# Kernel optimization log

Measured on AMD Instinct MI355X. Metric: run time of the kernel, lower is better.

## Reference

```python
import jax, jax.numpy as jnp
import numpy as np

N = 50000      # num_nodes
E = 1000000    # graph edges
EP = 400000    # pos/neg link-pred edges
H = 128        # hidden_dim
C = 768        # chemical_dim
L = 2          # num GCN layers


def setup_inputs() -> dict:
    key = jax.random.key(0)
    ks = jax.random.split(key, 12)
    edge_index = jax.random.randint(ks[0], (2, E), 0, N)
    chemistry = jax.random.normal(ks[1], (N, C), jnp.float32)
    pos_edge = jax.random.randint(ks[2], (EP, 2), 0, N)
    neg_edge = jax.random.randint(ks[3], (EP, 2), 0, N)
    smiles_mask = jax.random.uniform(ks[4], (N,), jnp.float32)
    node_emb = jax.random.normal(ks[5], (N, H), jnp.float32) * 0.1
    conv_w = jax.random.normal(ks[6], (L, H, H), jnp.float32) / np.sqrt(H)
    conv_b = jnp.zeros((L, H), jnp.float32)
    chem_w = jax.random.normal(ks[7], (C, H), jnp.float32) / np.sqrt(C)
    chem_b = jnp.zeros((H,), jnp.float32)
    dec_w1 = jax.random.normal(ks[8], (2 * H, H), jnp.float32) / np.sqrt(2 * H)
    dec_b1 = jnp.zeros((H,), jnp.float32)
    dec_w2 = jax.random.normal(ks[9], (H, 1), jnp.float32) / np.sqrt(H)
    dec_b2 = jnp.zeros((1,), jnp.float32)
    return dict(edge_index=edge_index, chemistry=chemistry, pos_edge=pos_edge,
                neg_edge=neg_edge, smiles_mask=smiles_mask, node_emb=node_emb,
                conv_w=conv_w, conv_b=conv_b, chem_w=chem_w, chem_b=chem_b,
                dec_w1=dec_w1, dec_b1=dec_b1, dec_w2=dec_w2, dec_b2=dec_b2)


def reference(edge_index, chemistry, pos_edge, neg_edge, smiles_mask, node_emb,
              conv_w, conv_b, chem_w, chem_b, dec_w1, dec_b1, dec_w2, dec_b2):
    row, col = edge_index[0], edge_index[1]  # src -> dst
    # GCN symmetric normalization (add_self_loops=False)
    deg = jax.ops.segment_sum(jnp.ones((E,), jnp.float32), col, num_segments=N)
    dinv = jnp.where(deg > 0, 1.0 / jnp.sqrt(jnp.maximum(deg, 1.0)), 0.0)
    norm = dinv[row] * dinv[col]  # [E]

    # Encoder: structure-only GCN over learned node embeddings
    z = node_emb
    for l in range(L):
        h = z @ conv_w[l]                       # [N,H]
        msg = h[row] * norm[:, None]            # gather [E,H]
        agg = jax.ops.segment_sum(msg, col, num_segments=N)  # scatter-add
        z = jax.nn.relu(agg + conv_b[l])

    # Chemistry projection, masked by smiles validity
    c = jax.nn.relu(chemistry @ chem_w + chem_b) * smiles_mask[:, None]  # [N,H]

    def decode(edges):
        src, dst = edges[:, 0], edges[:, 1]
        f = jnp.concatenate([z[src] * z[dst], c[src] * c[dst]], axis=-1)  # [Ep,2H]
        hmid = jax.nn.relu(f @ dec_w1 + dec_b1)
        return (hmid @ dec_w2 + dec_b2)[:, 0]

    return decode(pos_edge), decode(neg_edge)
```

## Files before the change

### kernel.cpp

```cpp
#include <hip/hip_runtime.h>
#include <hip/hip_fp16.h>

#define NN 50000
#define NE 1000000
#define NEP 400000
#define HD 128
#define CD 768
#define NB_SCAN 196
#define FSTR 256
#define NBKT 196
#define PBLK 2048
#define NPB ((2 * NEP + PBLK - 1) / PBLK)

typedef _Float16 f16x8 __attribute__((ext_vector_type(8)));
typedef _Float16 f16x2 __attribute__((ext_vector_type(2)));
typedef __fp16 hf16x2 __attribute__((ext_vector_type(2)));
typedef __attribute__((ext_vector_type(4))) float f32x4;

__device__ __forceinline__ unsigned pk2h(float a, float b) {
    hf16x2 p = __builtin_amdgcn_cvt_pkrtz(a, b);
    return __builtin_bit_cast(unsigned, p);
}
__device__ __forceinline__ ushort f2h(float x) {
    return (ushort)(pk2h(x, 0.f) & 0xffffu);
}
__device__ __forceinline__ unsigned h2mul(unsigned a, unsigned b) {
    f16x2 ha = __builtin_bit_cast(f16x2, a);
    f16x2 hb = __builtin_bit_cast(f16x2, b);
    f16x2 r = ha * hb;
    return __builtin_bit_cast(unsigned, r);
}
__device__ __forceinline__ f16x8 pack8h(float4 a0, float4 a1) {
    union { unsigned u[4]; f16x8 v; } r;
    r.u[0] = pk2h(a0.x, a0.y);
    r.u[1] = pk2h(a0.z, a0.w);
    r.u[2] = pk2h(a1.x, a1.y);
    r.u[3] = pk2h(a1.z, a1.w);
    return r.v;
}
__device__ __forceinline__ float2 h2f2(unsigned u) {
    f16x2 h = __builtin_bit_cast(f16x2, u);
    return make_float2((float)h[0], (float)h[1]);
}

__global__ __launch_bounds__(256) void count_kernel(const int* __restrict__ col,
                                                    int* __restrict__ cnt) {
    int i = blockIdx.x * 256 + threadIdx.x;
    if (i < NE) atomicAdd(&cnt[col[i]], 1);
}

__global__ __launch_bounds__(256) void scan1_kernel(const int* __restrict__ cnt,
                                                    int* __restrict__ partial,
                                                    int* __restrict__ bsum,
                                                    float* __restrict__ dinv) {
    __shared__ int s[256];
    int i = blockIdx.x * 256 + threadIdx.x;
    int v = (i < NN) ? cnt[i] : 0;
    if (i < NN) dinv[i] = (v > 0) ? 1.0f / sqrtf((float)v) : 0.0f;
    s[threadIdx.x] = v;
    __syncthreads();
    for (int o = 1; o < 256; o <<= 1) {
        int t = (threadIdx.x >= o) ? s[threadIdx.x - o] : 0;
        __syncthreads();
        s[threadIdx.x] += t;
        __syncthreads();
    }
    if (i < NN) partial[i] = s[threadIdx.x] - v;
    if (threadIdx.x == 255) bsum[blockIdx.x] = s[255];
}

__global__ __launch_bounds__(256) void scan2_kernel(int* __restrict__ bsum) {
    __shared__ int s[256];
    int v = (threadIdx.x < NB_SCAN) ? bsum[threadIdx.x] : 0;
    s[threadIdx.x] = v;
    __syncthreads();
    for (int o = 1; o < 256; o <<= 1) {
        int t = (threadIdx.x >= o) ? s[threadIdx.x - o] : 0;
        __syncthreads();
        s[threadIdx.x] += t;
        __syncthreads();
    }
    if (threadIdx.x < NB_SCAN) bsum[threadIdx.x] = s[threadIdx.x] - v;
}

__global__ __launch_bounds__(256) void scan3_kernel(const int* __restrict__ partial,
                                                    const int* __restrict__ bsum,
                                                    int* __restrict__ off,
                                                    int* __restrict__ cursor) {
    int i = blockIdx.x * 256 + threadIdx.x;
    if (i < NN) {
        int o = partial[i] + bsum[blockIdx.x];
        off[i] = o;
        cursor[i] = o;
    }
}

__global__ __launch_bounds__(256) void fill_kernel(const int* __restrict__ row,
                                                   const int* __restrict__ col,
                                                   const float* __restrict__ dinv,
                                                   int* __restrict__ cursor,
                                                   int* __restrict__ csr_idx,
                                                   float* __restrict__ csr_w) {
    int e = blockIdx.x * 256 + threadIdx.x;
    if (e < NE) {
        int c = col[e], r = row[e];
        int slot = atomicAdd(&cursor[c], 1);
        csr_idx[slot] = r;
        csr_w[slot] = dinv[r];
    }
}

__global__ __launch_bounds__(256) void ehist_kernel(const int* __restrict__ pos,
                                                    const int* __restrict__ neg,
                                                    int* __restrict__ bh,
                                                    int* __restrict__ bcnt) {
    __shared__ int h[NBKT];
    const int t = threadIdx.x;
    if (t < NBKT) h[t] = 0;
    __syncthreads();
    const int base = blockIdx.x * PBLK;
#pragma unroll
    for (int j = 0; j < 8; ++j) {
        int i = base + t + j * 256;
        if (i < 2 * NEP) {
            int s = (i < NEP) ? pos[2 * i] : neg[2 * (i - NEP)];
            atomicAdd(&h[s >> 8], 1);
        }
    }
    __syncthreads();
    if (t < NBKT) {
        bh[blockIdx.x * NBKT + t] = h[t];
        if (h[t]) atomicAdd(&bcnt[t], h[t]);
    }
}

__global__ __launch_bounds__(256) void escan_kernel(const int* __restrict__ bcnt,
                                                    int* __restrict__ base) {
    __shared__ int s[256];
    const int t = threadIdx.x;
    int v = (t < NBKT) ? bcnt[t] : 0;
    s[t] = v;
    __syncthreads();
    for (int o = 1; o < 256; o <<= 1) {
        int x = (t >= o) ? s[t - o] : 0;
        __syncthreads();
        s[t] += x;
        __syncthreads();
    }
    if (t < NBKT) base[t] = s[t] - v;
}

__global__ __launch_bounds__(256) void bscan_kernel(const int* __restrict__ bh,
                                                    int* __restrict__ obh) {
    __shared__ int p[256];
    const int b = blockIdx.x;
    const int t = threadIdx.x;
    int v0 = (2 * t < NPB) ? bh[(size_t)(2 * t) * NBKT + b] : 0;
    int v1 = (2 * t + 1 < NPB) ? bh[(size_t)(2 * t + 1) * NBKT + b] : 0;
    p[t] = v0 + v1;
    __syncthreads();
    for (int o = 1; o < 256; o <<= 1) {
        int x = (t >= o) ? p[t - o] : 0;
        __syncthreads();
        p[t] += x;
        __syncthreads();
    }
    int excl = (t > 0) ? p[t - 1] : 0;
    if (2 * t < NPB) obh[(size_t)(2 * t) * NBKT + b] = excl;
    if (2 * t + 1 < NPB) obh[(size_t)(2 * t + 1) * NBKT + b] = excl + v0;
}

__global__ __launch_bounds__(256) void epermute_kernel(const int* __restrict__ pos,
                                                       const int* __restrict__ neg,
                                                       const int* __restrict__ base,
                                                       const int* __restrict__ obh,
                                                       uint2* __restrict__ sd,
                                                       int* __restrict__ oidx) {
    __shared__ int cur[NBKT];
    const int t = threadIdx.x;
    if (t < NBKT) cur[t] = base[t] + obh[(size_t)blockIdx.x * NBKT + t];
    __syncthreads();
    const int bb = blockIdx.x * PBLK;
#pragma unroll
    for (int j = 0; j < 8; ++j) {
        int i = bb + t + j * 256;
        if (i < 2 * NEP) {
            int s, d;
            if (i < NEP) { s = pos[2 * i]; d = pos[2 * i + 1]; }
            else { s = neg[2 * (i - NEP)]; d = neg[2 * (i - NEP) + 1]; }
            int slot = atomicAdd(&cur[s >> 8], 1);
            sd[slot] = make_uint2((unsigned)s, (unsigned)d);
            oidx[slot] = i;
        }
    }
}

__global__ __launch_bounds__(256) void wfrag_all_kernel(const float* __restrict__ w1,
                                                        const float* __restrict__ wc,
                                                        const float* __restrict__ w0,
                                                        const float* __restrict__ wl1,
                                                        ushort* __restrict__ w1f,
                                                        ushort* __restrict__ wcf,
                                                        ushort* __restrict__ wc0f,
                                                        ushort* __restrict__ wc1f) {
    int tid = blockIdx.x * 256 + threadIdx.x;
    int g = tid >> 9;
    const float* w;
    ushort* wf;
    int ks;
    if (g < 8) { w = w1; wf = w1f; ks = g; }
    else if (g < 32) { w = wc; wf = wcf; ks = g - 8; }
    else if (g < 36) { w = w0; wf = wc0f; ks = g - 32; }
    else { w = wl1; wf = wc1f; ks = g - 36; }
    int nt = (tid >> 6) & 7, l = tid & 63;
    int kbase = ks * 32 + ((l >> 4) << 3);
    int colq = nt * 16 + (l & 15);
    ushort r[8];
#pragma unroll
    for (int j = 0; j < 8; ++j) r[j] = f2h(w[(size_t)(kbase + j) * HD + colq]);
    *(uint4*)&wf[(size_t)((ks * 8 + nt) * 64 + l) * 8] = *(uint4*)r;
}

template <int KS, bool EPI>
__global__ __launch_bounds__(256) void feat_mfma_kernel(const float* __restrict__ A,
                                                        const ushort* __restrict__ wf,
                                                        const float* __restrict__ bias,
                                                        const float* __restrict__ mask,
                                                        ushort* __restrict__ out,
                                                        int ostride, int ooff) {
    __shared__ float At[2][64][36];
    const int t = threadIdx.x;
    const int w = t >> 6, lane = t & 63;
    const int rowBase = blockIdx.x * 64;
    const int nt0 = w * 2;
    const int K = KS * 32;

    const int sr0 = t >> 3, sr1 = 32 + (t >> 3), sc4 = (t & 7) * 4;
    const int g0 = rowBase + sr0, g1 = rowBase + sr1;

    float4 p0 = make_float4(0.f, 0.f, 0.f, 0.f), p1 = p0;
    if (g0 < NN) p0 = *(const float4*)&A[(size_t)g0 * K + sc4];
    if (g1 < NN) p1 = *(const float4*)&A[(size_t)g1 * K + sc4];

    f32x4 acc[4][2] = {};

    for (int ks = 0; ks < KS; ++ks) {
        const int b = ks & 1;
        *(float4*)&At[b][sr0][sc4] = p0;
        *(float4*)&At[b][sr1][sc4] = p1;
        __syncthreads();
        if (ks + 1 < KS) {
            p0 = make_float4(0.f, 0.f, 0.f, 0.f); p1 = p0;
            if (g0 < NN) p0 = *(const float4*)&A[(size_t)g0 * K + (ks + 1) * 32 + sc4];
            if (g1 < NN) p1 = *(const float4*)&A[(size_t)g1 * K + (ks + 1) * 32 + sc4];
        }
        f16x8 bf0 = ((const f16x8*)wf)[(ks * 8 + nt0) * 64 + lane];
        f16x8 bf1 = ((const f16x8*)wf)[(ks * 8 + nt0 + 1) * 64 + lane];
#pragma unroll
        for (int mt = 0; mt < 4; ++mt) {
            int row = mt * 16 + (lane & 15);
            float4 a0 = *(const float4*)&At[b][row][(lane >> 4) * 8];
            float4 a1 = *(const float4*)&At[b][row][(lane >> 4) * 8 + 4];
            f16x8 af = pack8h(a0, a1);
            acc[mt][0] = __builtin_amdgcn_mfma_f32_16x16x32_f16(af, bf0, acc[mt][0], 0, 0, 0);
            acc[mt][1] = __builtin_amdgcn_mfma_f32_16x16x32_f16(af, bf1, acc[mt][1], 0, 0, 0);
        }
    }

    const int c0 = lane & 15, rq = lane >> 4;
    float bb0 = EPI ? bias[nt0 * 16 + c0] : 0.f;
    float bb1 = EPI ? bias[nt0 * 16 + 16 + c0] : 0.f;
#pragma unroll
    for (int mt = 0; mt < 4; ++mt) {
#pragma unroll
        for (int reg = 0; reg < 4; ++reg) {
            int grow = rowBase + mt * 16 + rq * 4 + reg;
            if (grow < NN) {
                float v0 = acc[mt][0][reg], v1 = acc[mt][1][reg];
                if (EPI) {
                    float m = mask[grow];
                    v0 = fmaxf(v0 + bb0, 0.f) * m;
                    v1 = fmaxf(v1 + bb1, 0.f) * m;
                }
                out[(size_t)grow * ostride + ooff + nt0 * 16 + c0] = f2h(v0);
                out[(size_t)grow * ostride + ooff + nt0 * 16 + 16 + c0] = f2h(v1);
            }
        }
    }
}

template <bool F16OUT>
__global__ __launch_bounds__(256) void gather_kernel(const int* __restrict__ off,
                                                     const int* __restrict__ cnt,
                                                     const int* __restrict__ csr_idx,
                                                     const float* __restrict__ csr_w,
                                                     const float* __restrict__ dinv,
                                                     const ushort* __restrict__ h,
                                                     const float* __restrict__ bias,
                                                     float* __restrict__ z,
                                                     ushort* __restrict__ zb,
                                                     int ostride) {
    int v = blockIdx.x * 4 + (threadIdx.x >> 6);
    if (v >= NN) return;
    int lane = threadIdx.x & 63;
    int s = off[v];
    int e = s + cnt[v];
    float accx = 0.f, accy = 0.f;
    for (; s + 7 < e; s += 8) {
        int r0 = csr_idx[s], r1 = csr_idx[s + 1], r2 = csr_idx[s + 2], r3 = csr_idx[s + 3];
        int r4 = csr_idx[s + 4], r5 = csr_idx[s + 5], r6 = csr_idx[s + 6], r7 = csr_idx[s + 7];
        unsigned u0 = *(const unsigned*)&h[(size_t)r0 * HD + lane * 2];
        unsigned u1 = *(const unsigned*)&h[(size_t)r1 * HD + lane * 2];
        unsigned u2 = *(const unsigned*)&h[(size_t)r2 * HD + lane * 2];
        unsigned u3 = *(const unsigned*)&h[(size_t)r3 * HD + lane * 2];
        unsigned u4 = *(const unsigned*)&h[(size_t)r4 * HD + lane * 2];
        unsigned u5 = *(const unsigned*)&h[(size_t)r5 * HD + lane * 2];
        unsigned u6 = *(const unsigned*)&h[(size_t)r6 * HD + lane * 2];
        unsigned u7 = *(const unsigned*)&h[(size_t)r7 * HD + lane * 2];
        float w0 = csr_w[s], w1 = csr_w[s + 1], w2 = csr_w[s + 2], w3 = csr_w[s + 3];
        float w4 = csr_w[s + 4], w5 = csr_w[s + 5], w6 = csr_w[s + 6], w7 = csr_w[s + 7];
        float2 f0 = h2f2(u0), f1 = h2f2(u1), f2 = h2f2(u2), f3 = h2f2(u3);
        float2 f4 = h2f2(u4), f5 = h2f2(u5), f6 = h2f2(u6), f7 = h2f2(u7);
        accx = fmaf(f0.x, w0, accx); accy = fmaf(f0.y, w0, accy);
        accx = fmaf(f1.x, w1, accx); accy = fmaf(f1.y, w1, accy);
        accx = fmaf(f2.x, w2, accx); accy = fmaf(f2.y, w2, accy);
        accx = fmaf(f3.x, w3, accx); accy = fmaf(f3.y, w3, accy);
        accx = fmaf(f4.x, w4, accx); accy = fmaf(f4.y, w4, accy);
        accx = fmaf(f5.x, w5, accx); accy = fmaf(f5.y, w5, accy);
        accx = fmaf(f6.x, w6, accx); accy = fmaf(f6.y, w6, accy);
        accx = fmaf(f7.x, w7, accx); accy = fmaf(f7.y, w7, accy);
    }
    for (; s < e; ++s) {
        int r0 = csr_idx[s];
        float w0 = csr_w[s];
        float2 f0 = h2f2(*(const unsigned*)&h[(size_t)r0 * HD + lane * 2]);
        accx = fmaf(f0.x, w0, accx); accy = fmaf(f0.y, w0, accy);
    }
    float dv = dinv[v];
    float2 b = *(const float2*)&bias[lane * 2];
    float ox = fmaxf(fmaf(accx, dv, b.x), 0.f);
    float oy = fmaxf(fmaf(accy, dv, b.y), 0.f);
    if (F16OUT) {
        *(unsigned*)&zb[(size_t)v * ostride + lane * 2] = pk2h(ox, oy);
    } else {
        float2 o; o.x = ox; o.y = oy;
        *(float2*)&z[(size_t)v * HD + lane * 2] = o;
    }
}

__global__ __launch_bounds__(256, 5) void decode_mfma_kernel(const uint2* __restrict__ sedges,
                                                             const int* __restrict__ soidx,
                                                             const ushort* __restrict__ feat,
                                                             const ushort* __restrict__ w1f,
                                                             const float* __restrict__ b1,
                                                             const float* __restrict__ w2,
                                                             const float* __restrict__ b2,
                                                             float* __restrict__ out) {
    __shared__ ushort Flds[8 * 4 * 64 * 8];
    const int t = threadIdx.x;
    const int w = t >> 6, lane = t & 63;

    const int nwg = gridDim.x;
    const int orig = blockIdx.x;
    const int q = nwg >> 3, r = nwg & 7;
    const int xcd = orig & 7, k = orig >> 3;
    const int wgid = (xcd < r ? xcd * (q + 1) : r * (q + 1) + (xcd - r) * q) + k;
    const int ebase = wgid * 64;

    const int seg = t & 31, eslot = t >> 5;
#pragma unroll
    for (int it = 0; it < 8; ++it) {
        int e = it * 8 + eslot;
        uint2 sd = sedges[ebase + e];
        uint4 av = *(const uint4*)&feat[(size_t)sd.x * FSTR + seg * 8];
        uint4 bv = *(const uint4*)&feat[(size_t)sd.y * FSTR + seg * 8];
        uint4 res;
        res.x = h2mul(av.x, bv.x);
        res.y = h2mul(av.y, bv.y);
        res.z = h2mul(av.z, bv.z);
        res.w = h2mul(av.w, bv.w);
        int ks = seg >> 2;
        int mt = e >> 4;
        int fl = (e & 15) | ((seg & 3) << 4);
        int swz = (seg & 3) | ((ks & 1) << 2);
        ((uint4*)Flds)[(ks * 4 + mt) * 64 + (fl ^ swz)] = res;
    }
    __syncthreads();

    f32x4 acc[4][2] = {};
    const int nt0 = w * 2;
#pragma unroll
    for (int ks = 0; ks < 8; ++ks) {
        f16x8 bf0 = ((const f16x8*)w1f)[(ks * 8 + nt0) * 64 + lane];
        f16x8 bf1 = ((const f16x8*)w1f)[(ks * 8 + nt0 + 1) * 64 + lane];
        const int rswz = ((lane >> 4) & 3) | ((ks & 1) << 2);
#pragma unroll
        for (int mt = 0; mt < 4; ++mt) {
            f16x8 af = ((const f16x8*)Flds)[(ks * 4 + mt) * 64 + (lane ^ rswz)];
            acc[mt][0] = __builtin_amdgcn_mfma_f32_16x16x32_f16(af, bf0, acc[mt][0], 0, 0, 0);
            acc[mt][1] = __builtin_amdgcn_mfma_f32_16x16x32_f16(af, bf1, acc[mt][1], 0, 0, 0);
        }
    }
    __syncthreads();

    float* partf = (float*)Flds;
    const int c0 = lane & 15, rq = lane >> 4;
    float b1v0 = b1[nt0 * 16 + c0], b1v1 = b1[nt0 * 16 + 16 + c0];
    float w2v0 = w2[nt0 * 16 + c0], w2v1 = w2[nt0 * 16 + 16 + c0];
#pragma unroll
    for (int mt = 0; mt < 4; ++mt) {
#pragma unroll
        for (int reg = 0; reg < 4; ++reg) {
            float h0 = fmaxf(acc[mt][0][reg] + b1v0, 0.f);
            float h1 = fmaxf(acc[mt][1][reg] + b1v1, 0.f);
            float p = fmaf(h0, w2v0, h1 * w2v1);
            p += __shfl_xor(p, 1);
            p += __shfl_xor(p, 2);
            p += __shfl_xor(p, 4);
            p += __shfl_xor(p, 8);
            if (c0 == 0) partf[w * 64 + mt * 16 + rq * 4 + reg] = p;
        }
    }
    __syncthreads();
    if (t < 64) {
        out[soidx[ebase + t]] = partf[t] + partf[64 + t] + partf[128 + t] + partf[192 + t] + b2[0];
    }
}

extern "C" void kernel_launch(void* const* d_in, const int* in_sizes, int n_in,
                              void* d_out, int out_size, void* d_ws, size_t ws_size,
                              hipStream_t stream) {
    const int* edge_index = (const int*)d_in[0];
    const float* chemistry = (const float*)d_in[1];
    const int* pos_edge = (const int*)d_in[2];
    const int* neg_edge = (const int*)d_in[3];
    const float* smiles_mask = (const float*)d_in[4];
    const float* node_emb = (const float*)d_in[5];
    const float* conv_w = (const float*)d_in[6];
    const float* conv_b = (const float*)d_in[7];
    const float* chem_w = (const float*)d_in[8];
    const float* chem_b = (const float*)d_in[9];
    const float* dec_w1 = (const float*)d_in[10];
    const float* dec_b1 = (const float*)d_in[11];
    const float* dec_w2 = (const float*)d_in[12];
    const float* dec_b2 = (const float*)d_in[13];
    float* out = (float*)d_out;

    char* ws = (char*)d_ws;
    int* cnt = (int*)(ws + 0);
    int* bcnt = (int*)(ws + 204800);
    float* dinv = (float*)(ws + 208896);
    int* partial = (int*)(ws + 409600);
    int* off = (int*)(ws + 614400);
    int* cursor = (int*)(ws + 819200);
    int* bsum = (int*)(ws + 1024000);
    int* bbase = (int*)(ws + 1026048);
    int* csr_idx = (int*)(ws + 1048576);
    float* csr_w = (float*)(ws + 5242880);
    float* bufZ = (float*)(ws + 9437184);
    ushort* hb = (ushort*)(ws + 35037184);
    ushort* feat = (ushort*)(ws + 47837184);
    ushort* w1f = (ushort*)(ws + 73437184);
    ushort* wcf = (ushort*)(ws + 73502720);
    ushort* wc0f = (ushort*)(ws + 73699328);
    ushort* wc1f = (ushort*)(ws + 73732096);
    uint2* sort_sd = (uint2*)(ws + 35037184);
    int* sort_oidx = (int*)(ws + 41437184);
    int* bh = (int*)(ws + 9437184);
    int* obh = (int*)(ws + 9857184);

    const int* e_row = edge_index;
    const int* e_col = edge_index + NE;

    hipMemsetAsync(ws, 0, 205824, stream);
    count_kernel<<<(NE + 255) / 256, 256, 0, stream>>>(e_col, cnt);
    scan1_kernel<<<NB_SCAN, 256, 0, stream>>>(cnt, partial, bsum, dinv);
    scan2_kernel<<<1, 256, 0, stream>>>(bsum);
    scan3_kernel<<<NB_SCAN, 256, 0, stream>>>(partial, bsum, off, cursor);
    fill_kernel<<<(NE + 255) / 256, 256, 0, stream>>>(e_row, e_col, dinv, cursor, csr_idx, csr_w);
    wfrag_all_kernel<<<80, 256, 0, stream>>>(dec_w1, chem_w, conv_w, conv_w + HD * HD,
                                             w1f, wcf, wc0f, wc1f);

    const int mmGrid = (NN + 63) / 64;
    const int gaGrid = (NN + 3) / 4;

    feat_mfma_kernel<4, false><<<mmGrid, 256, 0, stream>>>(node_emb, wc0f, nullptr, nullptr, hb, HD, 0);
    gather_kernel<false><<<gaGrid, 256, 0, stream>>>(off, cnt, csr_idx, csr_w, dinv, hb, conv_b, bufZ, nullptr, 0);

    feat_mfma_kernel<4, false><<<mmGrid, 256, 0, stream>>>(bufZ, wc1f, nullptr, nullptr, hb, HD, 0);
    gather_kernel<true><<<gaGrid, 256, 0, stream>>>(off, cnt, csr_idx, csr_w, dinv, hb, conv_b + HD, nullptr, feat, FSTR);

    ehist_kernel<<<NPB, 256, 0, stream>>>(pos_edge, neg_edge, bh, bcnt);
    escan_kernel<<<1, 256, 0, stream>>>(bcnt, bbase);
    bscan_kernel<<<NBKT, 256, 0, stream>>>(bh, obh);
    epermute_kernel<<<NPB, 256, 0, stream>>>(pos_edge, neg_edge, bbase, obh, sort_sd, sort_oidx);

    feat_mfma_kernel<24, true><<<mmGrid, 256, 0, stream>>>(chemistry, wcf, chem_b, smiles_mask, feat, FSTR, HD);

    decode_mfma_kernel<<<2 * NEP / 64, 256, 0, stream>>>(sort_sd, sort_oidx, feat, w1f,
                                                         dec_b1, dec_w2, dec_b2, out);
}
```

Baseline: 422.7 us.

## Store layer-1 GCN output in fp16 and prefetch decode gathers in batches

The first gather kernel now writes its output as fp16 instead of fp32. A new MFMA matmul kernel reads that fp16 activation directly, which halves the intermediate traffic and removes the fp32-to-fp16 conversion in the second layer's matmul. The decode kernel now issues all edge-index loads and then all feature gathers before any compute, using sched barriers to raise memory-level parallelism, and its occupancy hint drops from 5 to 4 to make room for the extra registers. Workspace offsets for the histogram buffers move to avoid overlapping the new fp16 buffer. The trade-off is a small precision loss in the intermediate activation.

```diff
diff --git a/kernel.cpp b/kernel.cpp
--- a/kernel.cpp
+++ b/kernel.cpp
@@ -289,7 +289,56 @@
     }
 }
 
-template <bool F16OUT>
+__global__ __launch_bounds__(256) void feat_mfma_f16a_kernel(const ushort* __restrict__ A,
+                                                             const ushort* __restrict__ wf,
+                                                             ushort* __restrict__ out) {
+    __shared__ ushort At[2][64][40];
+    const int t = threadIdx.x;
+    const int w = t >> 6, lane = t & 63;
+    const int rowBase = blockIdx.x * 64;
+    const int nt0 = w * 2;
+
+    const int sr = t >> 2, sc = (t & 3) * 8;
+    const int g = rowBase + sr;
+
+    uint4 p = make_uint4(0, 0, 0, 0);
+    if (g < NN) p = *(const uint4*)&A[(size_t)g * HD + sc];
+
+    f32x4 acc[4][2] = {};
+
+    for (int ks = 0; ks < 4; ++ks) {
+        const int b = ks & 1;
+        *(uint4*)&At[b][sr][sc] = p;
+        __syncthreads();
+        if (ks + 1 < 4) {
+            p = make_uint4(0, 0, 0, 0);
+            if (g < NN) p = *(const uint4*)&A[(size_t)g * HD + (ks + 1) * 32 + sc];
+        }
+        f16x8 bf0 = ((const f16x8*)wf)[(ks * 8 + nt0) * 64 + lane];
+        f16x8 bf1 = ((const f16x8*)wf)[(ks * 8 + nt0 + 1) * 64 + lane];
+#pragma unroll
+        for (int mt = 0; mt < 4; ++mt) {
+            int row = mt * 16 + (lane & 15);
+            f16x8 af = *(const f16x8*)&At[b][row][(lane >> 4) * 8];
+            acc[mt][0] = __builtin_amdgcn_mfma_f32_16x16x32_f16(af, bf0, acc[mt][0], 0, 0, 0);
+            acc[mt][1] = __builtin_amdgcn_mfma_f32_16x16x32_f16(af, bf1, acc[mt][1], 0, 0, 0);
+        }
+    }
+
+    const int c0 = lane & 15, rq = lane >> 4;
+#pragma unroll
+    for (int mt = 0; mt < 4; ++mt) {
+#pragma unroll
+        for (int reg = 0; reg < 4; ++reg) {
+            int grow = rowBase + mt * 16 + rq * 4 + reg;
+            if (grow < NN) {
+                out[(size_t)grow * HD + nt0 * 16 + c0] = f2h(acc[mt][0][reg]);
+                out[(size_t)grow * HD + nt0 * 16 + 16 + c0] = f2h(acc[mt][1][reg]);
+            }
+        }
+    }
+}
+
 __global__ __launch_bounds__(256) void gather_kernel(const int* __restrict__ off,
                                                      const int* __restrict__ cnt,
                                                      const int* __restrict__ csr_idx,
@@ -297,7 +346,6 @@
                                                      const float* __restrict__ dinv,
                                                      const ushort* __restrict__ h,
                                                      const float* __restrict__ bias,
-                                                     float* __restrict__ z,
                                                      ushort* __restrict__ zb,
                                                      int ostride) {
     int v = blockIdx.x * 4 + (threadIdx.x >> 6);
@@ -340,15 +388,10 @@
     float2 b = *(const float2*)&bias[lane * 2];
     float ox = fmaxf(fmaf(accx, dv, b.x), 0.f);
     float oy = fmaxf(fmaf(accy, dv, b.y), 0.f);
-    if (F16OUT) {
-        *(unsigned*)&zb[(size_t)v * ostride + lane * 2] = pk2h(ox, oy);
-    } else {
-        float2 o; o.x = ox; o.y = oy;
-        *(float2*)&z[(size_t)v * HD + lane * 2] = o;
-    }
-}
-
-__global__ __launch_bounds__(256, 5) void decode_mfma_kernel(const uint2* __restrict__ sedges,
+    *(unsigned*)&zb[(size_t)v * ostride + lane * 2] = pk2h(ox, oy);
+}
+
+__global__ __launch_bounds__(256, 4) void decode_mfma_kernel(const uint2* __restrict__ sedges,
                                                              const int* __restrict__ soidx,
                                                              const ushort* __restrict__ feat,
                                                              const ushort* __restrict__ w1f,
@@ -368,17 +411,26 @@
     const int ebase = wgid * 64;
 
     const int seg = t & 31, eslot = t >> 5;
-#pragma unroll
-    for (int it = 0; it < 8; ++it) {
-        int e = it * 8 + eslot;
-        uint2 sd = sedges[ebase + e];
-        uint4 av = *(const uint4*)&feat[(size_t)sd.x * FSTR + seg * 8];
-        uint4 bv = *(const uint4*)&feat[(size_t)sd.y * FSTR + seg * 8];
+
+    uint2 sdv[8];
+#pragma unroll
+    for (int j = 0; j < 8; ++j) sdv[j] = sedges[ebase + j * 8 + eslot];
+    __builtin_amdgcn_sched_barrier(0);
+    uint4 av[8], bv[8];
+#pragma unroll
+    for (int j = 0; j < 8; ++j) {
+        av[j] = *(const uint4*)&feat[(size_t)sdv[j].x * FSTR + seg * 8];
+        bv[j] = *(const uint4*)&feat[(size_t)sdv[j].y * FSTR + seg * 8];
+    }
+    __builtin_amdgcn_sched_barrier(0);
+#pragma unroll
+    for (int j = 0; j < 8; ++j) {
+        int e = j * 8 + eslot;
         uint4 res;
-        res.x = h2mul(av.x, bv.x);
-        res.y = h2mul(av.y, bv.y);
-        res.z = h2mul(av.z, bv.z);
-        res.w = h2mul(av.w, bv.w);
+        res.x = h2mul(av[j].x, bv[j].x);
+        res.y = h2mul(av[j].y, bv[j].y);
+        res.z = h2mul(av[j].z, bv[j].z);
+        res.w = h2mul(av[j].w, bv[j].w);
         int ks = seg >> 2;
         int mt = e >> 4;
         int fl = (e & 15) | ((seg & 3) << 4);
@@ -457,7 +509,9 @@
     int* bbase = (int*)(ws + 1026048);
     int* csr_idx = (int*)(ws + 1048576);
     float* csr_w = (float*)(ws + 5242880);
-    float* bufZ = (float*)(ws + 9437184);
+    ushort* bufZh = (ushort*)(ws + 9437184);
+    int* bh = (int*)(ws + 22237184);
+    int* obh = (int*)(ws + 22657184);
     ushort* hb = (ushort*)(ws + 35037184);
     ushort* feat = (ushort*)(ws + 47837184);
     ushort* w1f = (ushort*)(ws + 73437184);
@@ -466,8 +520,6 @@
     ushort* wc1f = (ushort*)(ws + 73732096);
     uint2* sort_sd = (uint2*)(ws + 35037184);
     int* sort_oidx = (int*)(ws + 41437184);
-    int* bh = (int*)(ws + 9437184);
-    int* obh = (int*)(ws + 9857184);
 
     const int* e_row = edge_index;
     const int* e_col = edge_index + NE;
@@ -485,10 +537,10 @@
     const int gaGrid = (NN + 3) / 4;
 
     feat_mfma_kernel<4, false><<<mmGrid, 256, 0, stream>>>(node_emb, wc0f, nullptr, nullptr, hb, HD, 0);
-    gather_kernel<false><<<gaGrid, 256, 0, stream>>>(off, cnt, csr_idx, csr_w, dinv, hb, conv_b, bufZ, nullptr, 0);
-
-    feat_mfma_kernel<4, false><<<mmGrid, 256, 0, stream>>>(bufZ, wc1f, nullptr, nullptr, hb, HD, 0);
-    gather_kernel<true><<<gaGrid, 256, 0, stream>>>(off, cnt, csr_idx, csr_w, dinv, hb, conv_b + HD, nullptr, feat, FSTR);
+    gather_kernel<<<gaGrid, 256, 0, stream>>>(off, cnt, csr_idx, csr_w, dinv, hb, conv_b, bufZh, HD);
+
+    feat_mfma_f16a_kernel<<<mmGrid, 256, 0, stream>>>(bufZh, wc1f, hb);
+    gather_kernel<<<gaGrid, 256, 0, stream>>>(off, cnt, csr_idx, csr_w, dinv, hb, conv_b + HD, feat, FSTR);
 
     ehist_kernel<<<NPB, 256, 0, stream>>>(pos_edge, neg_edge, bh, bcnt);
     escan_kernel<<<1, 256, 0, stream>>>(bcnt, bbase);
```

Measured after the change: 419.8 us. No clear change (-0.7%).
